# Kernel optimization log

Hardware: AMD Instinct MI355X
Metric: run time of the kernel (lower is better)

The kernel has to match this reference:

```python
import math
import jax, jax.numpy as jnp
import numpy as np

NH, D, MULT, VOCAB, NLAYER = 4, 256, 128, 256, 2
N = MULT * D // NH  # 8192
EPS = 1e-5
THETA = 2.0 ** 16


def get_freqs(n):
    q = (jnp.arange(n, dtype=jnp.float32) // 2) * 2  # quantize(t, 2)
    return 1.0 / (THETA ** (q / n)) / (2 * math.pi)


def ln(x):
    # LayerNorm over last dim, no affine
    mu = jnp.mean(x, axis=-1, keepdims=True)
    var = jnp.mean((x - mu) ** 2, axis=-1, keepdims=True)
    return (x - mu) / jnp.sqrt(var + EPS)


def rope(phases, v):
    # phases: (T, N), v: (B, nh, T, N)
    ph = (phases % 1.0) * (2 * math.pi)
    c, s = jnp.cos(ph), jnp.sin(ph)
    v_rot = jnp.stack((-v[..., 1::2], v[..., ::2]), axis=-1).reshape(v.shape)
    return v * c + v_rot * s


def setup_inputs() -> dict:
    key = jax.random.key(0)
    ks = jax.random.split(key, 6)
    std = 0.02
    return {
        "idx": jax.random.randint(ks[0], (1, 2048), 0, VOCAB),
        "embed": jax.random.normal(ks[1], (VOCAB, D), jnp.float32) * std,
        "encoder": jax.random.normal(ks[2], (NH, D, N), jnp.float32) * std,
        "encoder_v": jax.random.normal(ks[3], (NH, D, N), jnp.float32) * std,
        "decoder": jax.random.normal(ks[4], (NH * N, D), jnp.float32) * std,
        "lm_head": jax.random.normal(ks[5], (D, VOCAB), jnp.float32) * std,
    }


def reference(idx, embed, encoder, encoder_v, decoder, lm_head):
    B, T = idx.shape
    freqs = get_freqs(N)  # (N,)
    phases = jnp.arange(T, dtype=jnp.float32)[:, None] * freqs[None, :]  # (T, N)
    # strictly-lower-triangular causal mask (tril diagonal=-1)
    t = jnp.arange(T)
    mask = (t[:, None] > t[None, :]).astype(jnp.float32)  # (T, T)

    x = ln(embed[idx][:, None])  # (B, 1, T, D)
    for _ in range(NLAYER):
        x_sparse = jax.nn.relu(jnp.einsum('bltd,hdn->bhtn', x, encoder))  # (B,nh,T,N)
        QR = rope(phases, x_sparse)
        scores = jnp.einsum('bhtn,bhsn->bhts', QR, QR) * mask  # (B,nh,T,T)
        yKV = ln(jnp.einsum('bhts,blsd->bhtd', scores, x))  # (B,nh,T,D)
        y_sparse = jax.nn.relu(jnp.einsum('bhtd,hdn->bhtn', yKV, encoder_v))
        xy = x_sparse * y_sparse  # (B,nh,T,N)
        xy = xy.transpose(0, 2, 1, 3).reshape(B, 1, T, NH * N)
        yMLP = xy @ decoder  # (B,1,T,D)
        x = ln(x + ln(yMLP))
    logits = x[:, 0] @ lm_head  # (B,T,vocab)
    return logits
```

## Files before the change

### kernel.cpp

```cpp
#include <hip/hip_runtime.h>
#include <hip/hip_bf16.h>
#include <math.h>

typedef unsigned short u16;
typedef unsigned int u32;
typedef __attribute__((ext_vector_type(8))) short short8;
typedef __attribute__((ext_vector_type(4))) float f32x4;

__device__ __forceinline__ u16 f2b(float f) {
  u32 u = __builtin_bit_cast(u32, f);
  u = (u + 0x7fffu + ((u >> 16) & 1u)) >> 16;
  return (u16)u;
}
__device__ __forceinline__ float b2f(u16 s) {
  return __builtin_bit_cast(float, (u32)s << 16);
}

__device__ __forceinline__ void ld_g2l(const u16* g, u16* l) {
  __builtin_amdgcn_global_load_lds(
      (const __attribute__((address_space(1))) unsigned int*)g,
      (__attribute__((address_space(3))) unsigned int*)l, 16, 0, 0);
}

__device__ __forceinline__ void gemm_core(
    const u16* __restrict__ A, const u16* __restrict__ B,
    int lda, int ldb, int Klen, int kb, int bm, int bn,
    u16* __restrict__ As, u16* __restrict__ Bs, f32x4 (&acc)[4][4])
{
  int tid = threadIdx.x;
  int w = tid >> 6, lane = tid & 63;
  int srow = (w << 4) + (lane >> 2);
  int scol = (lane & 3) << 3;
  const u16* ga0 = A + (long)(bm * 128 + srow) * lda + kb + scol;
  const u16* ga1 = ga0 + (long)64 * lda;
  const u16* gb0 = B + (long)(bn * 128 + srow) * ldb + kb + scol;
  const u16* gb1 = gb0 + (long)64 * ldb;
  u16* la0 = As + (w << 9);  u16* la1 = la0 + 2048;
  u16* lb0 = Bs + (w << 9);  u16* lb1 = lb0 + 2048;

  int wm = (w >> 1) << 6, wn = (w & 1) << 6;
  int lane15 = lane & 15, quad = lane >> 4;
  const u16* ar = As + (wm + lane15) * 32 + quad * 8;
  const u16* br = Bs + (wn + lane15) * 32 + quad * 8;

#pragma unroll
  for (int i = 0; i < 4; i++)
#pragma unroll
    for (int j = 0; j < 4; j++) { f32x4 z = {0.f, 0.f, 0.f, 0.f}; acc[i][j] = z; }

  for (int k = 0; k < Klen; k += 32) {
    ld_g2l(ga0 + k, la0);
    ld_g2l(ga1 + k, la1);
    ld_g2l(gb0 + k, lb0);
    ld_g2l(gb1 + k, lb1);
    __syncthreads();
    short8 af[4], bfr[4];
#pragma unroll
    for (int mt = 0; mt < 4; mt++) af[mt] = *(const short8*)(ar + mt * 16 * 32);
#pragma unroll
    for (int nt = 0; nt < 4; nt++) bfr[nt] = *(const short8*)(br + nt * 16 * 32);
#pragma unroll
    for (int mt = 0; mt < 4; mt++)
#pragma unroll
      for (int nt = 0; nt < 4; nt++)
        acc[mt][nt] = __builtin_amdgcn_mfma_f32_16x16x32_bf16(af[mt], bfr[nt], acc[mt][nt], 0, 0, 0);
    __syncthreads();
  }
}

__device__ __forceinline__ void rope_cs(int n, int t, float& c, float& s) {
  float f = exp2f((float)(-(n & ~1)) * (1.0f / 512.0f)) * 0.15915494f;
  float ph = (float)t * f;
  ph -= floorf(ph);
  __sincosf(ph * 6.2831853f, &s, &c);
}

template<int EPI>
__global__ __launch_bounds__(256, 2) void gemm_bt(
    const u16* __restrict__ A, const u16* __restrict__ B, void* __restrict__ C,
    int K, int lda, int ldb, int ldc, int nsplits, long aB, long bB, long cB,
    int tri)
{
  __shared__ __align__(16) u16 As[128 * 32];
  __shared__ __align__(16) u16 Bs[128 * 32];
  int bn = blockIdx.x, bm = blockIdx.y;
  int batch = blockIdx.z / nsplits, sp = blockIdx.z % nsplits;
  int Klen = K / nsplits, kb = sp * Klen;
  if (tri) {
    int kend = (bm + 1) * 128;
    if (kb >= kend) return;
    if (kb + Klen > kend) Klen = kend - kb;
  }

  f32x4 acc[4][4];
  gemm_core(A + (long)batch * aB, B + (long)batch * bB, lda, ldb, Klen, kb, bm, bn, As, Bs, acc);

  int lane = threadIdx.x & 63, w = threadIdx.x >> 6;
  int wm = (w >> 1) << 6, wn = (w & 1) << 6;
  int lane15 = lane & 15, quad = lane >> 4;

#pragma unroll
  for (int mt = 0; mt < 4; mt++)
#pragma unroll
    for (int nt = 0; nt < 4; nt++) {
      int gn = bn * 128 + wn + nt * 16 + lane15;
#pragma unroll
      for (int r = 0; r < 4; r++) {
        int gm = bm * 128 + wm + mt * 16 + quad * 4 + r;
        float v = acc[mt][nt][r];
        long ci = (long)batch * cB + (long)gm * ldc + gn;
        if (EPI == 0) {
          ((float*)C)[ci] = v;
        } else if (EPI == 3) {
          atomicAdd(&((float*)C)[ci], v);
        }
      }
    }
}

#define SC_BAR   __builtin_amdgcn_s_barrier()
#define SC_LGKM0 asm volatile("s_waitcnt lgkmcnt(0)" ::: "memory")
#define SC_LGKM8 asm volatile("s_waitcnt lgkmcnt(8)" ::: "memory")
#define SC_VMF   do { asm volatile("s_waitcnt vmcnt(4)" ::: "memory"); \
                      __builtin_amdgcn_sched_barrier(0); } while (0)
#define SC_P1    __builtin_amdgcn_s_setprio(1)
#define SC_P0    __builtin_amdgcn_s_setprio(0)

#define DSA(Ab, mh) { \
  _Pragma("unroll") for (int mt = 0; mt < 4; mt++) { \
    aA[mt][0] = *(const short8*)((Ab) + ((mh) * 64 + mt * 16) * 64 + koff0); \
    aA[mt][1] = *(const short8*)((Ab) + ((mh) * 64 + mt * 16) * 64 + koff1); } }

#define DSB(Bb, nh, dst) { \
  _Pragma("unroll") for (int nt = 0; nt < 2; nt++) { \
    dst[nt][0] = *(const short8*)((Bb) + ((nh) * 32 + nt * 16) * 64 + koff0); \
    dst[nt][1] = *(const short8*)((Bb) + ((nh) * 32 + nt * 16) * 64 + koff1); } }

#define MMA(MH, NH, BB) { \
  _Pragma("unroll") for (int mt = 0; mt < 4; mt++) \
  _Pragma("unroll") for (int nt = 0; nt < 2; nt++) { \
    acc[(MH)*4+mt][(NH)*2+nt] = __builtin_amdgcn_mfma_f32_16x16x32_bf16( \
        aA[mt][0], BB[nt][0], acc[(MH)*4+mt][(NH)*2+nt], 0, 0, 0); \
    acc[(MH)*4+mt][(NH)*2+nt] = __builtin_amdgcn_mfma_f32_16x16x32_bf16( \
        aA[mt][1], BB[nt][1], acc[(MH)*4+mt][(NH)*2+nt], 0, 0, 0); } }

#define EIGHT_PHASE_LOOP(STGA, STGB) \
  for (int i = 0; i < nkt / 2; i++) { \
    int kt1 = 2 * i + 1; \
    int kt2 = 2 * i + 2; if (kt2 > nkt - 1) kt2 = nkt - 1; \
    int kt3 = 2 * i + 3; if (kt3 > nkt - 1) kt3 = nkt - 1; \
    short8 aA[4][2], bb0[2][2], bb1[2][2]; \
     \
    DSA(A0, 0); DSB(B0, 0, bb0); \
    STGA(gA, &Abuf[1][0], kt1); \
    SC_LGKM8; SC_BAR; SC_LGKM0; SC_P1; MMA(0, 0, bb0); SC_P0; SC_BAR; \
     \
    DSB(B0, 1, bb1); \
    STGA(gA + HSTEPA, &Abuf[1][128 * 64], kt1); \
    SC_BAR; SC_LGKM0; SC_P1; MMA(0, 1, bb1); SC_P0; SC_BAR; \
     \
    DSA(A0, 1); \
    STGB(gB, &Bbuf[0][0], kt2); \
    SC_BAR; SC_LGKM0; SC_P1; MMA(1, 1, bb1); SC_P0; SC_BAR; \
     \
    STGB(gB + HSTEPB, &Bbuf[0][128 * 64], kt2); \
    SC_VMF; SC_BAR; SC_LGKM0; SC_P1; MMA(1, 0, bb0); SC_P0; SC_BAR; \
     \
    DSA(A1, 0); DSB(B1, 0, bb0); \
    STGA(gA, &Abuf[0][0], kt2); \
    SC_LGKM8; SC_BAR; SC_LGKM0; SC_P1; MMA(0, 0, bb0); SC_P0; SC_BAR; \
     \
    DSB(B1, 1, bb1); \
    STGA(gA + HSTEPA, &Abuf[0][128 * 64], kt2); \
    SC_BAR; SC_LGKM0; SC_P1; MMA(0, 1, bb1); SC_P0; SC_BAR; \
     \
    DSA(A1, 1); \
    STGB(gB, &Bbuf[1][0], kt3); \
    SC_BAR; SC_LGKM0; SC_P1; MMA(1, 1, bb1); SC_P0; SC_BAR; \
     \
    STGB(gB + HSTEPB, &Bbuf[1][128 * 64], kt3); \
    SC_VMF; SC_BAR; SC_LGKM0; SC_P1; MMA(1, 0, bb0); SC_P0; SC_BAR; \
  }

__global__ __launch_bounds__(512, 1) void gemm_scores8(
    const u16* __restrict__ QR, u16* __restrict__ S, int T)
{
  __shared__ __align__(16) u16 Abuf[2][256 * 64];
  __shared__ __align__(16) u16 Bbuf[2][256 * 64];

  int q = blockIdx.x;
  int bm = (int)((sqrtf(8.f * (float)q + 1.f) - 1.f) * 0.5f);
  while ((bm + 1) * (bm + 2) / 2 <= q) bm++;
  while (bm * (bm + 1) / 2 > q) bm--;
  int bn = q - bm * (bm + 1) / 2;

  const u16* Q = QR + (long)blockIdx.z * (long)T * 8192;
  u16* Sb = S + (long)blockIdx.z * (long)T * T;

  int tid = threadIdx.x;
  int w = tid >> 6, lane = tid & 63;
  int wr = w >> 2, wc = w & 3;
  int lane15 = lane & 15, quad = lane >> 4;
  int swz = lane15 & 7;
  int koff0 = ((quad) ^ swz) << 3;
  int koff1 = ((4 + quad) ^ swz) << 3;

  const u16* gA = Q + (long)(bm * 256) * 8192;
  const u16* gB = Q + (long)(bn * 256) * 8192;

  const u16* A0 = &Abuf[0][(wr * 128 + lane15) * 64];
  const u16* A1 = &Abuf[1][(wr * 128 + lane15) * 64];
  const u16* B0 = &Bbuf[0][(wc * 64 + lane15) * 64];
  const u16* B1 = &Bbuf[1][(wc * 64 + lane15) * 64];

  int sr = lane >> 3, sc = lane & 7;
  long g_sk = (long)sr * 8192 + ((sc ^ sr) << 3);
  int l_base = (w * 16) * 64;
  long g_wrow = (long)(w * 16) * 8192;

  auto STG = [&](const u16* gHalfBase, u16* lHalfBase, int kt) {
    const u16* g = gHalfBase + g_wrow + g_sk + kt * 64;
    u16* l = lHalfBase + l_base;
    ld_g2l(g, l);
    ld_g2l(g + (long)8 * 8192, l + 8 * 64);
  };

  f32x4 acc[8][4];
#pragma unroll
  for (int i2 = 0; i2 < 8; i2++)
#pragma unroll
    for (int j = 0; j < 4; j++) { f32x4 z = {0.f, 0.f, 0.f, 0.f}; acc[i2][j] = z; }

  const long HSTEPA = (long)128 * 8192;
  const long HSTEPB = HSTEPA;

  STG(gA, &Abuf[0][0], 0); STG(gA + HSTEPA, &Abuf[0][128 * 64], 0);
  STG(gB, &Bbuf[0][0], 0); STG(gB + HSTEPB, &Bbuf[0][128 * 64], 0);
  STG(gB, &Bbuf[1][0], 1); STG(gB + HSTEPB, &Bbuf[1][128 * 64], 1);
  SC_VMF;
  SC_BAR;

  const int nkt = 8192 / 64;
  EIGHT_PHASE_LOOP(STG, STG)

#pragma unroll
  for (int mt = 0; mt < 8; mt++)
#pragma unroll
    for (int nt = 0; nt < 4; nt++) {
      int gn = bn * 256 + wc * 64 + nt * 16 + lane15;
#pragma unroll
      for (int r = 0; r < 4; r++) {
        int gm = bm * 256 + wr * 128 + mt * 16 + quad * 4 + r;
        Sb[(long)gm * T + gn] = f2b(gm > gn ? acc[mt][nt][r] : 0.f);
      }
    }
}

template<int EPI>
__global__ __launch_bounds__(512, 1) void gemm256_8ph(
    const u16* __restrict__ A, const u16* __restrict__ B, void* __restrict__ C,
    int K, int lda, int ldb, int ldc, int nsplits, long aB, long bB, long cB)
{
  __shared__ __align__(16) u16 Abuf[2][256 * 64];
  __shared__ __align__(16) u16 Bbuf[2][256 * 64];

  int bn = blockIdx.x, bm = blockIdx.y;
  int batch = blockIdx.z / nsplits, sp = blockIdx.z % nsplits;
  int Klen = K / nsplits, kb = sp * Klen;
  int nkt = Klen >> 6;

  int tid = threadIdx.x;
  int w = tid >> 6, lane = tid & 63;
  int wr = w >> 2, wc = w & 3;
  int lane15 = lane & 15, quad = lane >> 4;
  int swz = lane15 & 7;
  int koff0 = ((quad) ^ swz) << 3;
  int koff1 = ((4 + quad) ^ swz) << 3;

  const u16* gA = A + (long)batch * aB + (long)(bm * 256) * lda + kb;
  const u16* gB = B + (long)batch * bB + (long)(bn * 256) * ldb + kb;

  const u16* A0 = &Abuf[0][(wr * 128 + lane15) * 64];
  const u16* A1 = &Abuf[1][(wr * 128 + lane15) * 64];
  const u16* B0 = &Bbuf[0][(wc * 64 + lane15) * 64];
  const u16* B1 = &Bbuf[1][(wc * 64 + lane15) * 64];

  int sr = lane >> 3, sc = lane & 7;
  int l_base = (w * 16) * 64;
  long g_skA = (long)sr * lda + ((sc ^ sr) << 3);
  long g_skB = (long)sr * ldb + ((sc ^ sr) << 3);
  long g_wrowA = (long)(w * 16) * lda;
  long g_wrowB = (long)(w * 16) * ldb;
  const long HSTEPA = (long)128 * lda;
  const long HSTEPB = (long)128 * ldb;

  auto STGA = [&](const u16* gHalfBase, u16* lHalfBase, int kt) {
    const u16* g = gHalfBase + g_wrowA + g_skA + kt * 64;
    u16* l = lHalfBase + l_base;
    ld_g2l(g, l);
    ld_g2l(g + (long)8 * lda, l + 8 * 64);
  };
  auto STGB = [&](const u16* gHalfBase, u16* lHalfBase, int kt) {
    const u16* g = gHalfBase + g_wrowB + g_skB + kt * 64;
    u16* l = lHalfBase + l_base;
    ld_g2l(g, l);
    ld_g2l(g + (long)8 * ldb, l + 8 * 64);
  };

  f32x4 acc[8][4];
#pragma unroll
  for (int i2 = 0; i2 < 8; i2++)
#pragma unroll
    for (int j = 0; j < 4; j++) { f32x4 z = {0.f, 0.f, 0.f, 0.f}; acc[i2][j] = z; }

  STGA(gA, &Abuf[0][0], 0); STGA(gA + HSTEPA, &Abuf[0][128 * 64], 0);
  STGB(gB, &Bbuf[0][0], 0); STGB(gB + HSTEPB, &Bbuf[0][128 * 64], 0);
  STGB(gB, &Bbuf[1][0], 1); STGB(gB + HSTEPB, &Bbuf[1][128 * 64], 1);
  SC_VMF;
  SC_BAR;

  EIGHT_PHASE_LOOP(STGA, STGB)

#pragma unroll
  for (int mt = 0; mt < 8; mt++)
#pragma unroll
    for (int nt = 0; nt < 4; nt++) {
      int gn = bn * 256 + wc * 64 + nt * 16 + lane15;
#pragma unroll
      for (int r = 0; r < 4; r++) {
        int gm = bm * 256 + wr * 128 + mt * 16 + quad * 4 + r;
        float v = acc[mt][nt][r];
        long ci = (long)batch * cB + (long)gm * ldc + gn;
        if (EPI == 1) {
          float rv = fmaxf(v, 0.f);
          float ro = __shfl_xor(rv, 1);
          float c, s; rope_cs(gn, gm, c, s);
          float out = (gn & 1) ? (rv * c + ro * s) : (rv * c - ro * s);
          ((u16*)C)[ci] = f2b(out);
        } else if (EPI == 3) {
          atomicAdd(&((float*)C)[ci], v);
        } else if (EPI == 4) {
          u16* Cp = (u16*)C;
          float qv = b2f(Cp[ci]);
          float qo = __shfl_xor(qv, 1);
          float c, s; rope_cs(gn, gm, c, s);
          float xs = (gn & 1) ? (qv * c - qo * s) : (qv * c + qo * s);
          Cp[ci] = f2b(fmaxf(v, 0.f) * xs);
        }
      }
    }
}

__global__ __launch_bounds__(256) void trans_f32_bf16(
    const float* __restrict__ src, u16* __restrict__ dst, int R, int C)
{
  __shared__ float tile[32][33];
  long off = (long)blockIdx.z * R * C;
  const float* s = src + off;
  u16* d = dst + off;
  int lx = threadIdx.x & 31, ly = threadIdx.x >> 5;
  int c = blockIdx.x * 32 + lx;
#pragma unroll
  for (int p = 0; p < 32; p += 8)
    tile[ly + p][lx] = s[(long)(blockIdx.y * 32 + ly + p) * C + c];
  __syncthreads();
  int rr = blockIdx.y * 32 + lx;
#pragma unroll
  for (int p = 0; p < 32; p += 8)
    d[(long)(blockIdx.x * 32 + ly + p) * R + rr] = f2b(tile[lx][ly + p]);
}

__device__ __forceinline__ float block_sum(float v, float* red) {
#pragma unroll
  for (int o = 32; o > 0; o >>= 1) v += __shfl_down(v, o, 64);
  int lane = threadIdx.x & 63, wid = threadIdx.x >> 6;
  if (lane == 0) red[wid] = v;
  __syncthreads();
  float r = red[0] + red[1] + red[2] + red[3];
  __syncthreads();
  return r;
}

__global__ __launch_bounds__(256) void embed_ln(
    const int* __restrict__ idx, const float* __restrict__ embed,
    float* __restrict__ x, u16* __restrict__ xb, u16* __restrict__ xT, int T)
{
  __shared__ float red[4];
  int t = blockIdx.x, d = threadIdx.x;
  float v = embed[(long)idx[t] * 256 + d];
  float mu = block_sum(v, red) * (1.f / 256.f);
  float c = v - mu;
  float var = block_sum(c * c, red) * (1.f / 256.f);
  float o = c * rsqrtf(var + 1e-5f);
  x[(long)t * 256 + d] = o;
  xb[(long)t * 256 + d] = f2b(o);
  xT[(long)d * T + t] = f2b(o);
}

__global__ __launch_bounds__(256) void row_ln(
    const float* __restrict__ in, u16* __restrict__ out)
{
  __shared__ float red[4];
  long row = blockIdx.x;
  int d = threadIdx.x;
  float v = in[row * 256 + d];
  float mu = block_sum(v, red) * (1.f / 256.f);
  float c = v - mu;
  float var = block_sum(c * c, red) * (1.f / 256.f);
  out[row * 256 + d] = f2b(c * rsqrtf(var + 1e-5f));
}

__global__ __launch_bounds__(256) void resid_ln(
    const float* __restrict__ yMLP, float* __restrict__ x,
    u16* __restrict__ xb, u16* __restrict__ xT, int T)
{
  __shared__ float red[4];
  int t = blockIdx.x, d = threadIdx.x;
  float y = yMLP[(long)t * 256 + d];
  float mu1 = block_sum(y, red) * (1.f / 256.f);
  float c1 = y - mu1;
  float var1 = block_sum(c1 * c1, red) * (1.f / 256.f);
  float l1 = c1 * rsqrtf(var1 + 1e-5f);
  float v = x[(long)t * 256 + d] + l1;
  float mu2 = block_sum(v, red) * (1.f / 256.f);
  float c2 = v - mu2;
  float var2 = block_sum(c2 * c2, red) * (1.f / 256.f);
  float o = c2 * rsqrtf(var2 + 1e-5f);
  x[(long)t * 256 + d] = o;
  xb[(long)t * 256 + d] = f2b(o);
  xT[(long)d * T + t] = f2b(o);
}

extern "C" void kernel_launch(void* const* d_in, const int* in_sizes, int n_in,
                              void* d_out, int out_size, void* d_ws, size_t ws_size,
                              hipStream_t stream) {
  const int*   idx       = (const int*)d_in[0];
  const float* embed     = (const float*)d_in[1];
  const float* encoder   = (const float*)d_in[2];
  const float* encoder_v = (const float*)d_in[3];
  const float* decoder   = (const float*)d_in[4];
  const float* lm_head   = (const float*)d_in[5];
  const int T = in_sizes[0];
  const int D = 256, NH = 4, Nn = 8192, V = 256;

  char* ws = (char*)d_ws;
  size_t off = 0;
  auto alloc = [&](size_t bytes) -> void* {
    void* p = ws + off; off += (bytes + 255) & ~(size_t)255; return p;
  };
  float* x_f32   = (float*)alloc((size_t)T * D * 4);
  float* yMLP    = (float*)alloc((size_t)T * D * 4);
  float* yKV_f32 = (float*)alloc((size_t)NH * T * D * 4);
  u16* x_b    = (u16*)alloc((size_t)T * D * 2);
  u16* xT     = (u16*)alloc((size_t)T * D * 2);
  u16* yKV_b  = (u16*)alloc((size_t)NH * T * D * 2);
  u16* lmT    = (u16*)alloc((size_t)D * V * 2);
  u16* encT   = (u16*)alloc((size_t)NH * Nn * D * 2);
  u16* encvT  = (u16*)alloc((size_t)NH * Nn * D * 2);
  u16* decT   = (u16*)alloc((size_t)D * NH * Nn * 2);
  size_t per_head = ((size_t)T * T * 2 + 256) + ((size_t)T * Nn * 2 + 256);
  int HB = 4;
  while (HB > 1 && off + (size_t)HB * per_head > ws_size) HB >>= 1;
  u16* scores = (u16*)alloc((size_t)HB * T * T * 2);
  u16* QRxy   = (u16*)alloc((size_t)HB * T * Nn * 2);
  if (off > ws_size) return;

  trans_f32_bf16<<<dim3(Nn / 32, D / 32, NH), 256, 0, stream>>>(encoder, encT, D, Nn);
  trans_f32_bf16<<<dim3(Nn / 32, D / 32, NH), 256, 0, stream>>>(encoder_v, encvT, D, Nn);
  trans_f32_bf16<<<dim3(D / 32, (NH * Nn) / 32, 1), 256, 0, stream>>>(decoder, decT, NH * Nn, D);
  trans_f32_bf16<<<dim3(V / 32, D / 32, 1), 256, 0, stream>>>(lm_head, lmT, D, V);

  embed_ln<<<T, 256, 0, stream>>>(idx, embed, x_f32, x_b, xT, T);

  const int nbm = T / 256, ntri = nbm * (nbm + 1) / 2;

  for (int l = 0; l < 2; l++) {
    hipMemsetAsync(yMLP, 0, (size_t)T * D * 4, stream);
    for (int h0 = 0; h0 < NH; h0 += HB) {
      gemm256_8ph<1><<<dim3(Nn / 256, T / 256, HB), 512, 0, stream>>>(
          x_b, encT + (size_t)h0 * Nn * D, QRxy,
          D, D, D, Nn, 1, 0L, (long)Nn * D, (long)T * Nn);
      gemm_scores8<<<dim3(ntri, 1, HB), 512, 0, stream>>>(QRxy, scores, T);
      hipMemsetAsync(yKV_f32, 0, (size_t)HB * T * D * 4, stream);
      gemm_bt<3><<<dim3(D / 128, T / 128, HB * 8), 256, 0, stream>>>(
          scores, xT, yKV_f32,
          T, T, T, D, 8, (long)T * T, 0L, (long)T * D, 1);
      row_ln<<<HB * T, 256, 0, stream>>>(yKV_f32, yKV_b);
      gemm256_8ph<4><<<dim3(Nn / 256, T / 256, HB), 512, 0, stream>>>(
          yKV_b, encvT + (size_t)h0 * Nn * D, QRxy,
          D, D, D, Nn, 1, (long)T * D, (long)Nn * D, (long)T * Nn);
      gemm256_8ph<3><<<dim3(1, T / 256, HB * 8), 512, 0, stream>>>(
          QRxy, decT + (size_t)h0 * Nn, yMLP,
          Nn, Nn, NH * Nn, D, 8, (long)T * Nn, (long)Nn, 0L);
    }
    resid_ln<<<T, 256, 0, stream>>>(yMLP, x_f32, x_b, xT, T);
  }

  gemm_bt<0><<<dim3(V / 128, T / 128, 1), 256, 0, stream>>>(
      x_b, lmT, d_out, D, D, D, V, 1, 0L, 0L, 0L, 0);
}
```

Measured before the change: 1.303 ms.

## Move K=256 encoder GEMMs to 128-tile kernel, XCD-remap scores, widen K-step

```diff
diff --git a/kernel.cpp b/kernel.cpp
--- a/kernel.cpp
+++ b/kernel.cpp
@@ -20,6 +20,20 @@
   __builtin_amdgcn_global_load_lds(
       (const __attribute__((address_space(1))) unsigned int*)g,
       (__attribute__((address_space(3))) unsigned int*)l, 16, 0, 0);
+}
+
+__device__ __forceinline__ float rope_frev(int n) {
+  return exp2f((float)(-(n & ~1)) * (1.0f / 512.0f)) * 0.15915494f;
+}
+__device__ __forceinline__ void rope_cs_fast(float frev, int t, float& c, float& s) {
+  float ph = (float)t * frev;
+  ph -= floorf(ph);
+#if __has_builtin(__builtin_amdgcn_sinf) && __has_builtin(__builtin_amdgcn_cosf)
+  s = __builtin_amdgcn_sinf(ph);
+  c = __builtin_amdgcn_cosf(ph);
+#else
+  __sincosf(ph * 6.2831853f, &s, &c);
+#endif
 }
 
 __device__ __forceinline__ void gemm_core(
@@ -48,31 +62,31 @@
 #pragma unroll
     for (int j = 0; j < 4; j++) { f32x4 z = {0.f, 0.f, 0.f, 0.f}; acc[i][j] = z; }
 
-  for (int k = 0; k < Klen; k += 32) {
+  for (int k = 0; k < Klen; k += 64) {
     ld_g2l(ga0 + k, la0);
     ld_g2l(ga1 + k, la1);
     ld_g2l(gb0 + k, lb0);
     ld_g2l(gb1 + k, lb1);
+    ld_g2l(ga0 + k + 32, la0 + 4096);
+    ld_g2l(ga1 + k + 32, la1 + 4096);
+    ld_g2l(gb0 + k + 32, lb0 + 4096);
+    ld_g2l(gb1 + k + 32, lb1 + 4096);
     __syncthreads();
-    short8 af[4], bfr[4];
-#pragma unroll
-    for (int mt = 0; mt < 4; mt++) af[mt] = *(const short8*)(ar + mt * 16 * 32);
-#pragma unroll
-    for (int nt = 0; nt < 4; nt++) bfr[nt] = *(const short8*)(br + nt * 16 * 32);
-#pragma unroll
-    for (int mt = 0; mt < 4; mt++)
-#pragma unroll
-      for (int nt = 0; nt < 4; nt++)
-        acc[mt][nt] = __builtin_amdgcn_mfma_f32_16x16x32_bf16(af[mt], bfr[nt], acc[mt][nt], 0, 0, 0);
+#pragma unroll
+    for (int h = 0; h < 2; h++) {
+      short8 af[4], bfr[4];
+#pragma unroll
+      for (int mt = 0; mt < 4; mt++) af[mt] = *(const short8*)(ar + h * 4096 + mt * 16 * 32);
+#pragma unroll
+      for (int nt = 0; nt < 4; nt++) bfr[nt] = *(const short8*)(br + h * 4096 + nt * 16 * 32);
+#pragma unroll
+      for (int mt = 0; mt < 4; mt++)
+#pragma unroll
+        for (int nt = 0; nt < 4; nt++)
+          acc[mt][nt] = __builtin_amdgcn_mfma_f32_16x16x32_bf16(af[mt], bfr[nt], acc[mt][nt], 0, 0, 0);
+    }
     __syncthreads();
   }
-}
-
-__device__ __forceinline__ void rope_cs(int n, int t, float& c, float& s) {
-  float f = exp2f((float)(-(n & ~1)) * (1.0f / 512.0f)) * 0.15915494f;
-  float ph = (float)t * f;
-  ph -= floorf(ph);
-  __sincosf(ph * 6.2831853f, &s, &c);
 }
 
 template<int EPI>
@@ -81,8 +95,8 @@
     int K, int lda, int ldb, int ldc, int nsplits, long aB, long bB, long cB,
     int tri)
 {
-  __shared__ __align__(16) u16 As[128 * 32];
-  __shared__ __align__(16) u16 Bs[128 * 32];
+  __shared__ __align__(16) u16 As[2 * 128 * 32];
+  __shared__ __align__(16) u16 Bs[2 * 128 * 32];
   int bn = blockIdx.x, bm = blockIdx.y;
   int batch = blockIdx.z / nsplits, sp = blockIdx.z % nsplits;
   int Klen = K / nsplits, kb = sp * Klen;
@@ -99,6 +113,13 @@
   int wm = (w >> 1) << 6, wn = (w & 1) << 6;
   int lane15 = lane & 15, quad = lane >> 4;
 
+  float frev[4] = {0.f, 0.f, 0.f, 0.f};
+  if (EPI == 1 || EPI == 4) {
+#pragma unroll
+    for (int nt = 0; nt < 4; nt++)
+      frev[nt] = rope_frev(bn * 128 + wn + nt * 16 + lane15);
+  }
+
 #pragma unroll
   for (int mt = 0; mt < 4; mt++)
 #pragma unroll
@@ -111,8 +132,21 @@
         long ci = (long)batch * cB + (long)gm * ldc + gn;
         if (EPI == 0) {
           ((float*)C)[ci] = v;
+        } else if (EPI == 1) {
+          float rv = fmaxf(v, 0.f);
+          float ro = __shfl_xor(rv, 1);
+          float c, s; rope_cs_fast(frev[nt], gm, c, s);
+          float out = (gn & 1) ? (rv * c + ro * s) : (rv * c - ro * s);
+          ((u16*)C)[ci] = f2b(out);
         } else if (EPI == 3) {
           atomicAdd(&((float*)C)[ci], v);
+        } else if (EPI == 4) {
+          u16* Cp = (u16*)C;
+          float q = b2f(Cp[ci]);
+          float qo = __shfl_xor(q, 1);
+          float c, s; rope_cs_fast(frev[nt], gm, c, s);
+          float xs = (gn & 1) ? (q * c - qo * s) : (q * c + qo * s);
+          Cp[ci] = f2b(fmaxf(v, 0.f) * xs);
         }
       }
     }
@@ -183,19 +217,26 @@
   }
 
 __global__ __launch_bounds__(512, 1) void gemm_scores8(
-    const u16* __restrict__ QR, u16* __restrict__ S, int T)
+    const u16* __restrict__ QR, u16* __restrict__ S, int T, int ntri)
 {
   __shared__ __align__(16) u16 Abuf[2][256 * 64];
   __shared__ __align__(16) u16 Bbuf[2][256 * 64];
 
-  int q = blockIdx.x;
+  int total = gridDim.x;
+  int lin = blockIdx.x;
+  int cpx = total >> 3, rr = total & 7;
+  int xcd = lin & 7, ii = lin >> 3;
+  int c = (xcd < rr) ? xcd * (cpx + 1) + ii
+                     : rr * (cpx + 1) + (xcd - rr) * cpx + ii;
+  int zh = c / ntri, q = c % ntri;
+
   int bm = (int)((sqrtf(8.f * (float)q + 1.f) - 1.f) * 0.5f);
   while ((bm + 1) * (bm + 2) / 2 <= q) bm++;
   while (bm * (bm + 1) / 2 > q) bm--;
   int bn = q - bm * (bm + 1) / 2;
 
-  const u16* Q = QR + (long)blockIdx.z * (long)T * 8192;
-  u16* Sb = S + (long)blockIdx.z * (long)T * T;
+  const u16* Q = QR + (long)zh * (long)T * 8192;
+  u16* Sb = S + (long)zh * (long)T * T;
 
   int tid = threadIdx.x;
   int w = tid >> 6, lane = tid & 63;
@@ -331,21 +372,10 @@
         int gm = bm * 256 + wr * 128 + mt * 16 + quad * 4 + r;
         float v = acc[mt][nt][r];
         long ci = (long)batch * cB + (long)gm * ldc + gn;
-        if (EPI == 1) {
-          float rv = fmaxf(v, 0.f);
-          float ro = __shfl_xor(rv, 1);
-          float c, s; rope_cs(gn, gm, c, s);
-          float out = (gn & 1) ? (rv * c + ro * s) : (rv * c - ro * s);
-          ((u16*)C)[ci] = f2b(out);
-        } else if (EPI == 3) {
+        if (EPI == 3) {
           atomicAdd(&((float*)C)[ci], v);
-        } else if (EPI == 4) {
-          u16* Cp = (u16*)C;
-          float qv = b2f(Cp[ci]);
-          float qo = __shfl_xor(qv, 1);
-          float c, s; rope_cs(gn, gm, c, s);
-          float xs = (gn & 1) ? (qv * c - qo * s) : (qv * c + qo * s);
-          Cp[ci] = f2b(fmaxf(v, 0.f) * xs);
+        } else {
+          ((float*)C)[ci] = v;
         }
       }
     }
@@ -477,18 +507,18 @@
   for (int l = 0; l < 2; l++) {
     hipMemsetAsync(yMLP, 0, (size_t)T * D * 4, stream);
     for (int h0 = 0; h0 < NH; h0 += HB) {
-      gemm256_8ph<1><<<dim3(Nn / 256, T / 256, HB), 512, 0, stream>>>(
+      gemm_bt<1><<<dim3(Nn / 128, T / 128, HB), 256, 0, stream>>>(
           x_b, encT + (size_t)h0 * Nn * D, QRxy,
-          D, D, D, Nn, 1, 0L, (long)Nn * D, (long)T * Nn);
-      gemm_scores8<<<dim3(ntri, 1, HB), 512, 0, stream>>>(QRxy, scores, T);
+          D, D, D, Nn, 1, 0L, (long)Nn * D, (long)T * Nn, 0);
+      gemm_scores8<<<dim3(ntri * HB, 1, 1), 512, 0, stream>>>(QRxy, scores, T, ntri);
       hipMemsetAsync(yKV_f32, 0, (size_t)HB * T * D * 4, stream);
-      gemm_bt<3><<<dim3(D / 128, T / 128, HB * 8), 256, 0, stream>>>(
+      gemm_bt<3><<<dim3(D / 128, T / 128, HB * 4), 256, 0, stream>>>(
           scores, xT, yKV_f32,
-          T, T, T, D, 8, (long)T * T, 0L, (long)T * D, 1);
+          T, T, T, D, 4, (long)T * T, 0L, (long)T * D, 1);
       row_ln<<<HB * T, 256, 0, stream>>>(yKV_f32, yKV_b);
-      gemm256_8ph<4><<<dim3(Nn / 256, T / 256, HB), 512, 0, stream>>>(
+      gemm_bt<4><<<dim3(Nn / 128, T / 128, HB), 256, 0, stream>>>(
           yKV_b, encvT + (size_t)h0 * Nn * D, QRxy,
-          D, D, D, Nn, 1, (long)T * D, (long)Nn * D, (long)T * Nn);
+          D, D, D, Nn, 1, (long)T * D, (long)Nn * D, (long)T * Nn, 0);
       gemm256_8ph<3><<<dim3(1, T / 256, HB * 8), 512, 0, stream>>>(
           QRxy, decT + (size_t)h0 * Nn, yMLP,
           Nn, Nn, NH * Nn, D, 8, (long)T * Nn, (long)Nn, 0L);
```

Measured after the change: 1.151 ms. -11.7%, faster.
